# Optimization experiments

Measured on AMD Instinct MI355X. Metric: run time of the kernel, lower is better.

Reference implementation:

```python
import jax, jax.numpy as jnp
import numpy as np

NUM_USERS = 50000
NUM_ITEMS = 50000
N_NODES = NUM_USERS + NUM_ITEMS
NNZ = 3200000
EMB_DIM = 64
N_LAYERS = 3
BATCH = 16384


def setup_inputs() -> dict:
    key = jax.random.key(0)
    ks = jax.random.split(key, 7)
    user_emb = 0.1 * jax.random.normal(ks[0], (NUM_USERS, EMB_DIM), dtype=jnp.float32)
    item_emb = 0.1 * jax.random.normal(ks[1], (NUM_ITEMS, EMB_DIM), dtype=jnp.float32)
    edge_val = jax.random.uniform(ks[2], (NNZ,), dtype=jnp.float32)
    edge_src = jax.random.randint(ks[3], (NNZ,), 0, N_NODES, dtype=jnp.int32)
    edge_dst = jax.random.randint(ks[4], (NNZ,), 0, N_NODES, dtype=jnp.int32)
    users = jax.random.randint(ks[5], (BATCH,), 0, NUM_USERS, dtype=jnp.int32)
    items = jax.random.randint(ks[6], (BATCH,), 0, NUM_ITEMS, dtype=jnp.int32)
    return {"user_emb": user_emb, "item_emb": item_emb, "edge_val": edge_val,
            "edge_src": edge_src, "edge_dst": edge_dst, "users": users, "items": items}


def _computer(user_emb, item_emb, edge_val, edge_src, edge_dst):
    # LightGCN propagation: all_emb <- A @ all_emb, mean over layer outputs (incl. layer 0)
    all_emb = jnp.concatenate([user_emb, item_emb], axis=0)  # [N, D]
    acc = all_emb
    for _ in range(N_LAYERS):
        msg = edge_val[:, None] * all_emb[edge_src]          # [nnz, D]
        all_emb = jax.ops.segment_sum(msg, edge_dst, num_segments=N_NODES)
        acc = acc + all_emb
    light_out = acc / jnp.float32(N_LAYERS + 1)
    return light_out[:NUM_USERS], light_out[NUM_USERS:]


def reference(user_emb, item_emb, edge_val, edge_src, edge_dst, users, items):
    all_users, all_items = _computer(user_emb, item_emb, edge_val, edge_src, edge_dst)
    users_emb = all_users[users]                              # [B, D]
    items_emb = all_items[items]                              # [B, D]
    gamma = jnp.sum(users_emb * items_emb, axis=1)            # [B]
    return gamma
```

## Files before the change

kernel.cpp:

```cpp
#include <hip/hip_runtime.h>

#define NUM_USERS 50000
#define NUM_ITEMS 50000
#define N_NODES   100000
#define NNZ       3200000
#define EMB_DIM   64
#define N_LAYERS  3
#define BATCH     16384

#define NBUCK 512
#define ABITS 8
#define NODES_PER_BUCK 256
#define TILE_EDGES 8192
#define NBUCK_USED ((N_NODES + NODES_PER_BUCK - 1) / NODES_PER_BUCK)
#define CAP 9216
#define BM_WORDS ((N_NODES + 31) / 32)

typedef unsigned long long ull;

__device__ inline unsigned bf16pair(float a, float b) {
    unsigned ua = __float_as_uint(a), ub = __float_as_uint(b);
    unsigned r0 = (ua + 0x7fffu + ((ua >> 16) & 1u)) >> 16;
    unsigned r1 = (ub + 0x7fffu + ((ub >> 16) & 1u)) >> 16;
    return r0 | (r1 << 16);
}

__device__ inline void acc8(float* s, uint4 g, float w) {
    s[0] = fmaf(w, __uint_as_float(g.x << 16),        s[0]);
    s[1] = fmaf(w, __uint_as_float(g.x & 0xffff0000u), s[1]);
    s[2] = fmaf(w, __uint_as_float(g.y << 16),        s[2]);
    s[3] = fmaf(w, __uint_as_float(g.y & 0xffff0000u), s[3]);
    s[4] = fmaf(w, __uint_as_float(g.z << 16),        s[4]);
    s[5] = fmaf(w, __uint_as_float(g.z & 0xffff0000u), s[5]);
    s[6] = fmaf(w, __uint_as_float(g.w << 16),        s[6]);
    s[7] = fmaf(w, __uint_as_float(g.w & 0xffff0000u), s[7]);
}

__global__ void init_emb_kernel(const float* __restrict__ ue,
                                const float* __restrict__ ie,
                                unsigned* __restrict__ bufA16,
                                float* __restrict__ acc,
                                int* __restrict__ bucketCursor,
                                unsigned* __restrict__ bitmap) {
    int idx = blockIdx.x * blockDim.x + threadIdx.x;
    if (blockIdx.x == 0) {
        if (threadIdx.x < 256) {
            bucketCursor[threadIdx.x]       = threadIdx.x * CAP;
            bucketCursor[threadIdx.x + 256] = (threadIdx.x + 256) * CAP;
        }
        for (int i = threadIdx.x; i < BM_WORDS; i += 256) bitmap[i] = 0;
    }
    const int total = N_NODES * (EMB_DIM / 4);
    if (idx >= total) return;
    const int uoff = NUM_USERS * (EMB_DIM / 4);
    float4 v;
    if (idx < uoff) v = ((const float4*)ue)[idx];
    else            v = ((const float4*)ie)[idx - uoff];
    ((float4*)acc)[idx] = v;
    uint2 h;
    h.x = bf16pair(v.x, v.y);
    h.y = bf16pair(v.z, v.w);
    ((uint2*)bufA16)[idx] = h;
}

__global__ void flag_kernel(const int* __restrict__ users,
                            const int* __restrict__ items,
                            unsigned* __restrict__ bitmap) {
    int t = blockIdx.x * blockDim.x + threadIdx.x;
    if (t < BATCH) {
        int n = users[t];
        atomicOr(&bitmap[n >> 5], 1u << (n & 31));
    } else if (t < 2 * BATCH) {
        int n = NUM_USERS + items[t - BATCH];
        atomicOr(&bitmap[n >> 5], 1u << (n & 31));
    }
}

__global__ void partA_kernel(const float* __restrict__ ev,
                             const int*  __restrict__ es,
                             const int*  __restrict__ ed,
                             int* __restrict__ bucketCursor,
                             ull* __restrict__ tmp) {
    __shared__ int hist[NBUCK];
    __shared__ int base[NBUCK];
    __shared__ int cnt2[NBUCK];
    int tid = threadIdx.x;
    int e0 = blockIdx.x * TILE_EDGES;

    int      mySrc[8], myDst[8];
    unsigned myQ[8];

    for (int i = tid; i < NBUCK; i += 1024) hist[i] = 0;
    __syncthreads();

    #pragma unroll
    for (int k = 0; k < 8; ++k) {
        int e = e0 + k * 1024 + tid;
        if (e < NNZ) {
            mySrc[k] = es[e];
            myDst[k] = ed[e];
            myQ[k]   = (unsigned)fminf(ev[e] * 32768.f + 0.5f, 32767.f);
            atomicAdd(&hist[((unsigned)myDst[k]) >> ABITS], 1);
        } else {
            myDst[k] = -1;
        }
    }
    __syncthreads();

    for (int i = tid; i < NBUCK; i += 1024) {
        int c = hist[i];
        base[i] = c ? atomicAdd(&bucketCursor[i], c) : 0;
        cnt2[i] = 0;
    }
    __syncthreads();

    #pragma unroll
    for (int k = 0; k < 8; ++k) {
        int dst = myDst[k];
        if (dst < 0) continue;
        int b = ((unsigned)dst) >> ABITS;
        int pos = base[b] + atomicAdd(&cnt2[b], 1);
        if (pos < (b + 1) * CAP) {
            ull rec = (ull)(unsigned)(mySrc[k] | ((dst & (NODES_PER_BUCK - 1)) << 17))
                    | ((ull)myQ[k] << 25);
            tmp[pos] = rec;
        }
    }
}

__global__ void partB_kernel(const ull* __restrict__ tmp,
                             const int* __restrict__ bucketCursor,
                             int* __restrict__ rowStart,
                             int* __restrict__ deg,
                             unsigned* __restrict__ sorted) {
    __shared__ int cnt[NODES_PER_BUCK];
    __shared__ int sc[NODES_PER_BUCK];
    __shared__ int cur[NODES_PER_BUCK];
    int b = blockIdx.x;
    int tid = threadIdx.x;
    int nodeLo = b << ABITS;
    int startE = b * CAP;
    int endE   = bucketCursor[b];

    if (tid < NODES_PER_BUCK) cnt[tid] = 0;
    __syncthreads();

    ull myRec[9];
    int nRec = 0;
    #pragma unroll
    for (int k = 0; k < 9; ++k) {
        int i = startE + k * 1024 + tid;
        if (i < endE) {
            myRec[k] = tmp[i];
            nRec = k + 1;
            atomicAdd(&cnt[(int)((myRec[k] >> 17) & (NODES_PER_BUCK - 1))], 1);
        }
    }
    __syncthreads();

    if (tid < NODES_PER_BUCK) sc[tid] = cnt[tid];
    __syncthreads();
    for (int o = 1; o < NODES_PER_BUCK; o <<= 1) {
        int add = 0;
        if (tid < NODES_PER_BUCK && tid >= o) add = sc[tid - o];
        __syncthreads();
        if (tid < NODES_PER_BUCK) sc[tid] += add;
        __syncthreads();
    }
    if (tid < NODES_PER_BUCK) {
        int node = nodeLo + tid;
        int rs = startE + sc[tid] - cnt[tid];
        cur[tid] = rs;
        if (node < N_NODES) {
            rowStart[node] = rs;
            deg[node] = cnt[tid];
        }
    }
    __syncthreads();

    for (int k = 0; k < nRec; ++k) {
        ull rec = myRec[k];
        int dl = (int)((rec >> 17) & (NODES_PER_BUCK - 1));
        unsigned o = (unsigned)(rec & 0x1FFFFULL) | ((unsigned)((rec >> 25) & 0x7FFF) << 17);
        int pos = atomicAdd(&cur[dl], 1);
        sorted[pos] = o;
    }
}

__global__ void pull_kernel(const uint4* __restrict__ A16,
                            uint4* __restrict__ B16,
                            float* __restrict__ acc,
                            const unsigned* __restrict__ sorted,
                            const int* __restrict__ rowStart,
                            const int* __restrict__ deg,
                            const unsigned* __restrict__ bitmap,
                            int writeB, int gate) {
    int t = blockIdx.x * blockDim.x + threadIdx.x;
    int node = t >> 6;
    if (node >= N_NODES) return;
    if (gate && !((bitmap[node >> 5] >> (node & 31)) & 1u)) return;
    int lane = t & 63;
    int eg = lane >> 3;
    int d8 = lane & 7;
    int start = rowStart[node];
    int cnt   = deg[node];
    const unsigned* ep = sorted + start;
    const float k15 = 1.f / 32768.f;

    float s[8] = {0.f,0.f,0.f,0.f,0.f,0.f,0.f,0.f};
    int j = 0;
    while (j + 32 <= cnt) {
        unsigned r0 = ep[j + eg], r1 = ep[j + 8 + eg];
        unsigned r2 = ep[j + 16 + eg], r3 = ep[j + 24 + eg];
        uint4 g0 = A16[(((long long)(r0 & 0x1FFFFu)) << 3) + d8];
        uint4 g1 = A16[(((long long)(r1 & 0x1FFFFu)) << 3) + d8];
        uint4 g2 = A16[(((long long)(r2 & 0x1FFFFu)) << 3) + d8];
        uint4 g3 = A16[(((long long)(r3 & 0x1FFFFu)) << 3) + d8];
        acc8(s, g0, (float)(r0 >> 17) * k15);
        acc8(s, g1, (float)(r1 >> 17) * k15);
        acc8(s, g2, (float)(r2 >> 17) * k15);
        acc8(s, g3, (float)(r3 >> 17) * k15);
        j += 32;
    }
    while (j + 16 <= cnt) {
        unsigned r0 = ep[j + eg], r1 = ep[j + 8 + eg];
        uint4 g0 = A16[(((long long)(r0 & 0x1FFFFu)) << 3) + d8];
        uint4 g1 = A16[(((long long)(r1 & 0x1FFFFu)) << 3) + d8];
        acc8(s, g0, (float)(r0 >> 17) * k15);
        acc8(s, g1, (float)(r1 >> 17) * k15);
        j += 16;
    }
    for (; j < cnt; j += 8) {
        int idx = j + eg;
        unsigned r = (idx < cnt) ? ep[idx] : 0u;
        uint4 g = A16[(((long long)(r & 0x1FFFFu)) << 3) + d8];
        acc8(s, g, (float)(r >> 17) * k15);
    }
    #pragma unroll
    for (int k = 0; k < 8; ++k) {
        s[k] += __shfl_xor(s[k], 8, 64);
        s[k] += __shfl_xor(s[k], 16, 64);
        s[k] += __shfl_xor(s[k], 32, 64);
    }
    if (eg == 0) {
        float4* C4 = (float4*)acc;
        long long o = ((long long)node << 4) + d8 * 2;
        float4 c0 = C4[o], c1 = C4[o + 1];
        c0.x += s[0]; c0.y += s[1]; c0.z += s[2]; c0.w += s[3];
        c1.x += s[4]; c1.y += s[5]; c1.z += s[6]; c1.w += s[7];
        C4[o] = c0; C4[o + 1] = c1;
        if (writeB) {
            uint4 h;
            h.x = bf16pair(s[0], s[1]);
            h.y = bf16pair(s[2], s[3]);
            h.z = bf16pair(s[4], s[5]);
            h.w = bf16pair(s[6], s[7]);
            B16[(((long long)node) << 3) + d8] = h;
        }
    }
}

__global__ void dot_kernel(const float* __restrict__ acc,
                           const int* __restrict__ users,
                           const int* __restrict__ items,
                           float* __restrict__ out) {
    int t = blockIdx.x * blockDim.x + threadIdx.x;
    int b = t >> 6;
    int d = t & 63;
    if (b >= BATCH) return;
    int u  = users[b];
    int it = items[b] + NUM_USERS;
    float p = acc[(long long)u * EMB_DIM + d] * acc[(long long)it * EMB_DIM + d];
    #pragma unroll
    for (int off = 32; off >= 1; off >>= 1)
        p += __shfl_down(p, off, 64);
    if (d == 0) out[b] = p * 0.0625f;
}

extern "C" void kernel_launch(void* const* d_in, const int* in_sizes, int n_in,
                              void* d_out, int out_size, void* d_ws, size_t ws_size,
                              hipStream_t stream) {
    const float* user_emb = (const float*)d_in[0];
    const float* item_emb = (const float*)d_in[1];
    const float* edge_val = (const float*)d_in[2];
    const int*   edge_src = (const int*)d_in[3];
    const int*   edge_dst = (const int*)d_in[4];
    const int*   users    = (const int*)d_in[5];
    const int*   items    = (const int*)d_in[6];
    float* out = (float*)d_out;

    const size_t emb16Bytes = (size_t)N_NODES * EMB_DIM * 2;
    const size_t embBytes   = (size_t)N_NODES * EMB_DIM * sizeof(float);
    const size_t sortBytes  = (size_t)NBUCK_USED * CAP * sizeof(unsigned);
    const size_t tmpBytes   = (size_t)NBUCK_USED * CAP * sizeof(ull);
    const size_t nodeBytes  = (size_t)N_NODES * sizeof(int);

    char* w = (char*)d_ws;
    unsigned* bufA16       = (unsigned*)(w); w += emb16Bytes;
    unsigned* bufB16       = (unsigned*)(w); w += emb16Bytes;
    float*    acc          = (float*)(w);    w += embBytes;
    unsigned* sorted       = (unsigned*)(w); w += sortBytes;
    ull*      tmp          = (ull*)(w);      w += tmpBytes;
    int*      deg          = (int*)(w);      w += nodeBytes;
    int*      rowStart     = (int*)(w);      w += nodeBytes;
    int*      bucketCursor = (int*)(w);      w += NBUCK * sizeof(int);
    unsigned* bitmap       = (unsigned*)(w); w += BM_WORDS * sizeof(unsigned);

    const int vecTotal   = N_NODES * (EMB_DIM / 4);
    const int initBlocks = (vecTotal + 255) / 256;
    const int tileBlocks = (NNZ + TILE_EDGES - 1) / TILE_EDGES;

    init_emb_kernel<<<initBlocks, 256, 0, stream>>>(user_emb, item_emb,
                                                    bufA16, acc, bucketCursor, bitmap);
    flag_kernel<<<(2 * BATCH + 255) / 256, 256, 0, stream>>>(users, items, bitmap);

    partA_kernel<<<tileBlocks, 1024, 0, stream>>>(edge_val, edge_src, edge_dst,
                                                  bucketCursor, tmp);
    partB_kernel<<<NBUCK_USED, 1024, 0, stream>>>(tmp, bucketCursor,
                                                  rowStart, deg, sorted);

    const int pullBlocks = (N_NODES * 64 + 255) / 256;
    for (int layer = 0; layer < N_LAYERS; ++layer) {
        int last = (layer == N_LAYERS - 1);
        pull_kernel<<<pullBlocks, 256, 0, stream>>>((const uint4*)bufA16, (uint4*)bufB16,
                                                    acc, sorted, rowStart, deg, bitmap,
                                                    last ? 0 : 1, last ? 1 : 0);
        unsigned* tswap = bufA16; bufA16 = bufB16; bufB16 = tswap;
    }

    const int dotBlocks = (BATCH * 64 + 255) / 256;
    dot_kernel<<<dotBlocks, 256, 0, stream>>>(acc, users, items, out);
}
```

Baseline: 307.9 us.

## Drop fp32 accumulator; keep per-layer bf16 buffers and sum layers in dot kernel

```diff
diff --git a/kernel.cpp b/kernel.cpp
--- a/kernel.cpp
+++ b/kernel.cpp
@@ -24,22 +24,19 @@
     unsigned r1 = (ub + 0x7fffu + ((ub >> 16) & 1u)) >> 16;
     return r0 | (r1 << 16);
 }
+__device__ inline float blo(unsigned u) { return __uint_as_float(u << 16); }
+__device__ inline float bhi(unsigned u) { return __uint_as_float(u & 0xffff0000u); }
 
 __device__ inline void acc8(float* s, uint4 g, float w) {
-    s[0] = fmaf(w, __uint_as_float(g.x << 16),        s[0]);
-    s[1] = fmaf(w, __uint_as_float(g.x & 0xffff0000u), s[1]);
-    s[2] = fmaf(w, __uint_as_float(g.y << 16),        s[2]);
-    s[3] = fmaf(w, __uint_as_float(g.y & 0xffff0000u), s[3]);
-    s[4] = fmaf(w, __uint_as_float(g.z << 16),        s[4]);
-    s[5] = fmaf(w, __uint_as_float(g.z & 0xffff0000u), s[5]);
-    s[6] = fmaf(w, __uint_as_float(g.w << 16),        s[6]);
-    s[7] = fmaf(w, __uint_as_float(g.w & 0xffff0000u), s[7]);
+    s[0] = fmaf(w, blo(g.x), s[0]); s[1] = fmaf(w, bhi(g.x), s[1]);
+    s[2] = fmaf(w, blo(g.y), s[2]); s[3] = fmaf(w, bhi(g.y), s[3]);
+    s[4] = fmaf(w, blo(g.z), s[4]); s[5] = fmaf(w, bhi(g.z), s[5]);
+    s[6] = fmaf(w, blo(g.w), s[6]); s[7] = fmaf(w, bhi(g.w), s[7]);
 }
 
 __global__ void init_emb_kernel(const float* __restrict__ ue,
                                 const float* __restrict__ ie,
-                                unsigned* __restrict__ bufA16,
-                                float* __restrict__ acc,
+                                unsigned* __restrict__ E0,
                                 int* __restrict__ bucketCursor,
                                 unsigned* __restrict__ bitmap) {
     int idx = blockIdx.x * blockDim.x + threadIdx.x;
@@ -56,11 +53,10 @@
     float4 v;
     if (idx < uoff) v = ((const float4*)ue)[idx];
     else            v = ((const float4*)ie)[idx - uoff];
-    ((float4*)acc)[idx] = v;
     uint2 h;
     h.x = bf16pair(v.x, v.y);
     h.y = bf16pair(v.z, v.w);
-    ((uint2*)bufA16)[idx] = h;
+    ((uint2*)E0)[idx] = h;
 }
 
 __global__ void flag_kernel(const int* __restrict__ users,
@@ -189,12 +185,11 @@
 
 __global__ void pull_kernel(const uint4* __restrict__ A16,
                             uint4* __restrict__ B16,
-                            float* __restrict__ acc,
                             const unsigned* __restrict__ sorted,
                             const int* __restrict__ rowStart,
                             const int* __restrict__ deg,
                             const unsigned* __restrict__ bitmap,
-                            int writeB, int gate) {
+                            int gate) {
     int t = blockIdx.x * blockDim.x + threadIdx.x;
     int node = t >> 6;
     if (node >= N_NODES) return;
@@ -243,38 +238,39 @@
         s[k] += __shfl_xor(s[k], 32, 64);
     }
     if (eg == 0) {
-        float4* C4 = (float4*)acc;
-        long long o = ((long long)node << 4) + d8 * 2;
-        float4 c0 = C4[o], c1 = C4[o + 1];
-        c0.x += s[0]; c0.y += s[1]; c0.z += s[2]; c0.w += s[3];
-        c1.x += s[4]; c1.y += s[5]; c1.z += s[6]; c1.w += s[7];
-        C4[o] = c0; C4[o + 1] = c1;
-        if (writeB) {
-            uint4 h;
-            h.x = bf16pair(s[0], s[1]);
-            h.y = bf16pair(s[2], s[3]);
-            h.z = bf16pair(s[4], s[5]);
-            h.w = bf16pair(s[6], s[7]);
-            B16[(((long long)node) << 3) + d8] = h;
-        }
-    }
-}
-
-__global__ void dot_kernel(const float* __restrict__ acc,
+        uint4 h;
+        h.x = bf16pair(s[0], s[1]);
+        h.y = bf16pair(s[2], s[3]);
+        h.z = bf16pair(s[4], s[5]);
+        h.w = bf16pair(s[6], s[7]);
+        B16[(((long long)node) << 3) + d8] = h;
+    }
+}
+
+__global__ void dot_kernel(const unsigned* __restrict__ E0,
+                           const unsigned* __restrict__ B1,
+                           const unsigned* __restrict__ B2,
+                           const unsigned* __restrict__ B3,
                            const int* __restrict__ users,
                            const int* __restrict__ items,
                            float* __restrict__ out) {
     int t = blockIdx.x * blockDim.x + threadIdx.x;
-    int b = t >> 6;
-    int d = t & 63;
+    int b = t >> 5;
+    int lane = t & 31;
     if (b >= BATCH) return;
-    int u  = users[b];
-    int it = items[b] + NUM_USERS;
-    float p = acc[(long long)u * EMB_DIM + d] * acc[(long long)it * EMB_DIM + d];
-    #pragma unroll
-    for (int off = 32; off >= 1; off >>= 1)
-        p += __shfl_down(p, off, 64);
-    if (d == 0) out[b] = p * 0.0625f;
+    long long uo = ((long long)users[b] << 5) + lane;
+    long long io = ((long long)(items[b] + NUM_USERS) << 5) + lane;
+    unsigned a0 = E0[uo], a1 = B1[uo], a2 = B2[uo], a3 = B3[uo];
+    unsigned c0 = E0[io], c1 = B1[io], c2 = B2[io], c3 = B3[io];
+    float ux = (blo(a0) + blo(a1)) + (blo(a2) + blo(a3));
+    float uy = (bhi(a0) + bhi(a1)) + (bhi(a2) + bhi(a3));
+    float ix = (blo(c0) + blo(c1)) + (blo(c2) + blo(c3));
+    float iy = (bhi(c0) + bhi(c1)) + (bhi(c2) + bhi(c3));
+    float p = ux * ix + uy * iy;
+    #pragma unroll
+    for (int off = 16; off >= 1; off >>= 1)
+        p += __shfl_xor(p, off, 64);
+    if (lane == 0) out[b] = p * 0.0625f;
 }
 
 extern "C" void kernel_launch(void* const* d_in, const int* in_sizes, int n_in,
@@ -290,15 +286,15 @@
     float* out = (float*)d_out;
 
     const size_t emb16Bytes = (size_t)N_NODES * EMB_DIM * 2;
-    const size_t embBytes   = (size_t)N_NODES * EMB_DIM * sizeof(float);
     const size_t sortBytes  = (size_t)NBUCK_USED * CAP * sizeof(unsigned);
     const size_t tmpBytes   = (size_t)NBUCK_USED * CAP * sizeof(ull);
     const size_t nodeBytes  = (size_t)N_NODES * sizeof(int);
 
     char* w = (char*)d_ws;
-    unsigned* bufA16       = (unsigned*)(w); w += emb16Bytes;
-    unsigned* bufB16       = (unsigned*)(w); w += emb16Bytes;
-    float*    acc          = (float*)(w);    w += embBytes;
+    unsigned* E0           = (unsigned*)(w); w += emb16Bytes;
+    unsigned* B1           = (unsigned*)(w); w += emb16Bytes;
+    unsigned* B2           = (unsigned*)(w); w += emb16Bytes;
+    unsigned* B3           = (unsigned*)(w); w += emb16Bytes;
     unsigned* sorted       = (unsigned*)(w); w += sortBytes;
     ull*      tmp          = (ull*)(w);      w += tmpBytes;
     int*      deg          = (int*)(w);      w += nodeBytes;
@@ -311,7 +307,7 @@
     const int tileBlocks = (NNZ + TILE_EDGES - 1) / TILE_EDGES;
 
     init_emb_kernel<<<initBlocks, 256, 0, stream>>>(user_emb, item_emb,
-                                                    bufA16, acc, bucketCursor, bitmap);
+                                                    E0, bucketCursor, bitmap);
     flag_kernel<<<(2 * BATCH + 255) / 256, 256, 0, stream>>>(users, items, bitmap);
 
     partA_kernel<<<tileBlocks, 1024, 0, stream>>>(edge_val, edge_src, edge_dst,
@@ -320,14 +316,13 @@
                                                   rowStart, deg, sorted);
 
     const int pullBlocks = (N_NODES * 64 + 255) / 256;
-    for (int layer = 0; layer < N_LAYERS; ++layer) {
-        int last = (layer == N_LAYERS - 1);
-        pull_kernel<<<pullBlocks, 256, 0, stream>>>((const uint4*)bufA16, (uint4*)bufB16,
-                                                    acc, sorted, rowStart, deg, bitmap,
-                                                    last ? 0 : 1, last ? 1 : 0);
-        unsigned* tswap = bufA16; bufA16 = bufB16; bufB16 = tswap;
-    }
-
-    const int dotBlocks = (BATCH * 64 + 255) / 256;
-    dot_kernel<<<dotBlocks, 256, 0, stream>>>(acc, users, items, out);
-}
+    pull_kernel<<<pullBlocks, 256, 0, stream>>>((const uint4*)E0, (uint4*)B1,
+                                                sorted, rowStart, deg, bitmap, 0);
+    pull_kernel<<<pullBlocks, 256, 0, stream>>>((const uint4*)B1, (uint4*)B2,
+                                                sorted, rowStart, deg, bitmap, 0);
+    pull_kernel<<<pullBlocks, 256, 0, stream>>>((const uint4*)B2, (uint4*)B3,
+                                                sorted, rowStart, deg, bitmap, 1);
+
+    const int dotBlocks = (BATCH * 32 + 255) / 256;
+    dot_kernel<<<dotBlocks, 256, 0, stream>>>(E0, B1, B2, B3, users, items, out);
+}
```

After: 287.6 us. -6.6%, faster.
